# Optimization experiments

Hardware: AMD Instinct MI355X
Metric: run time of the kernel (lower is better)

## Reference

```python
import jax, jax.numpy as jnp
import numpy as np

VOCAB = 50257
D_MODEL = 128
BATCH = 4096
WINDOW = 5  # 2*WINDOW context ids per center word


def setup_inputs() -> dict:
    key = jax.random.key(0)
    k1, k2, k3, k4 = jax.random.split(key, 4)
    context_ids = jax.random.randint(k1, (BATCH, 2 * WINDOW), 0, VOCAB, dtype=jnp.int64 if jax.config.jax_enable_x64 else jnp.int32)
    center_ids = jax.random.randint(k2, (BATCH,), 0, VOCAB, dtype=jnp.int64 if jax.config.jax_enable_x64 else jnp.int32)
    emb = jax.random.normal(k3, (VOCAB, D_MODEL), dtype=jnp.float32)
    W = jax.random.normal(k4, (VOCAB, D_MODEL), dtype=jnp.float32)
    return {"context_ids": context_ids, "center_ids": center_ids, "emb": emb, "W": W}


def reference(context_ids, center_ids, emb, W):
    # CBOW: gather context embeddings, average over the window, project to vocab.
    ctx = emb[context_ids]                      # [B, 2W, D]
    cbow = ctx.mean(axis=1)                     # [B, D]
    logits = jnp.einsum("bd,vd->bv", cbow, W)   # [B, V]
    # CrossEntropyLoss (mean reduction) against center ids.
    logp = jax.nn.log_softmax(logits, axis=-1)  # [B, V]
    nll = -jnp.take_along_axis(logp, center_ids[:, None], axis=-1)[:, 0]
    loss = nll.mean()
    return loss
```

## Files before the change

kernel.cpp:

```cpp
#include <hip/hip_runtime.h>
#include <hip/hip_bf16.h>
#include <math.h>

#define VOCAB 50257
#define VPAD  50304
#define DMODEL 128
#define BATCH 4096
#define NW 10
#define LOG2E 1.4426950408889634f

typedef __bf16 bf16_t;
typedef __bf16 bf16x4 __attribute__((ext_vector_type(4)));
typedef __bf16 bf16x8 __attribute__((ext_vector_type(8)));
typedef float  floatx4 __attribute__((ext_vector_type(4)));

#if __has_builtin(__builtin_amdgcn_exp2f)
#define EXP2(x) __builtin_amdgcn_exp2f(x)
#else
#define EXP2(x) exp2f(x)
#endif

typedef const __attribute__((address_space(1))) void* gvp;
typedef __attribute__((address_space(3))) void* svp;

#define PREP_CBOW_BLOCKS 512
#define PREP_WCONV_BLOCKS 3144

__global__ void k_prep(const int* __restrict__ ctx, const int* __restrict__ center,
                       const float* __restrict__ emb, const float* __restrict__ W,
                       bf16_t* __restrict__ cbow_bf, bf16_t* __restrict__ Wb,
                       float* __restrict__ center_logit, float* __restrict__ sumexp) {
    const int tid = threadIdx.x;
    if (blockIdx.x < PREP_CBOW_BLOCKS) {
        const int g32 = tid >> 5;
        const int l32 = tid & 31;
        const int b = blockIdx.x * 8 + g32;
        const int* cr = ctx + b * NW;
        float4 s = make_float4(0.f, 0.f, 0.f, 0.f);
#pragma unroll
        for (int w = 0; w < NW; ++w) {
            const int id = cr[w];
            float4 v = *reinterpret_cast<const float4*>(emb + (long)id * DMODEL + l32 * 4);
            s.x += v.x; s.y += v.y; s.z += v.z; s.w += v.w;
        }
        s.x *= 0.1f; s.y *= 0.1f; s.z *= 0.1f; s.w *= 0.1f;
        bf16x4 o;
        o[0] = (bf16_t)(s.x * LOG2E); o[1] = (bf16_t)(s.y * LOG2E);
        o[2] = (bf16_t)(s.z * LOG2E); o[3] = (bf16_t)(s.w * LOG2E);
        *reinterpret_cast<bf16x4*>(cbow_bf + b * DMODEL + l32 * 4) = o;

        const int cid = center[b];
        float4 wv = *reinterpret_cast<const float4*>(W + (long)cid * DMODEL + l32 * 4);
        float p = s.x * wv.x + s.y * wv.y + s.z * wv.z + s.w * wv.w;
#pragma unroll
        for (int off = 16; off >= 1; off >>= 1) p += __shfl_xor(p, off, 64);
        if (l32 == 0) {
            center_logit[b] = p;
            sumexp[b] = 0.f;
        }
    } else {
        const long base = ((long)(blockIdx.x - PREP_CBOW_BLOCKS) * 256 + tid) * 8;
        bf16x8 o;
        if (base < (long)VOCAB * DMODEL) {
            float4 a = *reinterpret_cast<const float4*>(W + base);
            float4 b = *reinterpret_cast<const float4*>(W + base + 4);
            o[0] = (bf16_t)a.x; o[1] = (bf16_t)a.y; o[2] = (bf16_t)a.z; o[3] = (bf16_t)a.w;
            o[4] = (bf16_t)b.x; o[5] = (bf16_t)b.y; o[6] = (bf16_t)b.z; o[7] = (bf16_t)b.w;
        } else {
            o = (bf16x8)(bf16_t)0.f;
        }
        *reinterpret_cast<bf16x8*>(Wb + base) = o;
    }
}

#define BM 256
#define BN 128
#define NTILES 393
#define NSPLIT 32

__device__ __forceinline__ void stage_tile(const bf16_t* __restrict__ Wb,
                                           bf16_t* bs, int n0, int wv, int l15, int q) {
#pragma unroll
    for (int i = 0; i < 8; ++i) {
        const int f = wv * 8 + i;
        const int nf = f >> 2, ks = f & 3;
        const bf16_t* g = Wb + (long)(n0 + nf * 16 + l15) * DMODEL + ks * 32 + q * 8;
        __builtin_amdgcn_global_load_lds((gvp)g, (svp)(bs + f * 512), 16, 0, 0);
    }
}

template<bool MASKED>
__device__ __forceinline__ void compute_tile(const bf16_t* bs,
                                             const bf16x8 (&afrag)[4][4],
                                             float (&ssum)[4][4],
                                             int n0, int lane, int l15) {
#pragma unroll
    for (int nf = 0; nf < 8; ++nf) {
        const bf16_t* bp = bs + nf * 2048 + lane * 8;
        bf16x8 b0 = *reinterpret_cast<const bf16x8*>(bp);
        bf16x8 b1 = *reinterpret_cast<const bf16x8*>(bp + 512);
        bf16x8 b2 = *reinterpret_cast<const bf16x8*>(bp + 1024);
        bf16x8 b3 = *reinterpret_cast<const bf16x8*>(bp + 1536);

        floatx4 acc[4];
#pragma unroll
        for (int mf = 0; mf < 4; ++mf) acc[mf] = (floatx4){0.f, 0.f, 0.f, 0.f};
#pragma unroll
        for (int mf = 0; mf < 4; ++mf)
            acc[mf] = __builtin_amdgcn_mfma_f32_16x16x32_bf16(afrag[mf][0], b0, acc[mf], 0, 0, 0);
#pragma unroll
        for (int mf = 0; mf < 4; ++mf)
            acc[mf] = __builtin_amdgcn_mfma_f32_16x16x32_bf16(afrag[mf][1], b1, acc[mf], 0, 0, 0);
#pragma unroll
        for (int mf = 0; mf < 4; ++mf)
            acc[mf] = __builtin_amdgcn_mfma_f32_16x16x32_bf16(afrag[mf][2], b2, acc[mf], 0, 0, 0);
#pragma unroll
        for (int mf = 0; mf < 4; ++mf)
            acc[mf] = __builtin_amdgcn_mfma_f32_16x16x32_bf16(afrag[mf][3], b3, acc[mf], 0, 0, 0);

        const bool ok = !MASKED || ((n0 + nf * 16 + l15) < VOCAB);
#pragma unroll
        for (int mf = 0; mf < 4; ++mf) {
#pragma unroll
            for (int r = 0; r < 4; ++r) {
                float e = EXP2(acc[mf][r]);
                ssum[mf][r] += ok ? e : 0.f;
            }
        }
    }
}

__launch_bounds__(256, 2)
__global__ void k_gemm(const bf16_t* __restrict__ A, const bf16_t* __restrict__ Wb,
                       float* __restrict__ sumexp) {
    __shared__ bf16_t Bs[2][32 * 512];
    const int tid  = threadIdx.x;
    const int lane = tid & 63;
    const int wv   = tid >> 6;
    const int l15  = lane & 15;
    const int q    = lane >> 4;
    const int m0   = blockIdx.x * BM;
    const int by   = blockIdx.y;

    stage_tile(Wb, &Bs[0][0], by * BN, wv, l15, q);

    bf16x8 afrag[4][4];
#pragma unroll
    for (int mf = 0; mf < 4; ++mf) {
        const bf16_t* ap = A + (long)(m0 + wv * 64 + mf * 16 + l15) * DMODEL + q * 8;
#pragma unroll
        for (int ks = 0; ks < 4; ++ks)
            afrag[mf][ks] = *reinterpret_cast<const bf16x8*>(ap + ks * 32);
    }

    float ssum[4][4];
#pragma unroll
    for (int mf = 0; mf < 4; ++mf)
#pragma unroll
        for (int r = 0; r < 4; ++r) ssum[mf][r] = 0.f;

    asm volatile("s_waitcnt vmcnt(0)" ::: "memory");
    __builtin_amdgcn_s_barrier();
    __builtin_amdgcn_sched_barrier(0);

    int cur = 0;
    for (int nt = by; nt < NTILES; nt += NSPLIT) {
        const int nnext = nt + NSPLIT;
        if (nnext < NTILES)
            stage_tile(Wb, &Bs[cur ^ 1][0], nnext * BN, wv, l15, q);

        const int n0 = nt * BN;
        const bf16_t* bs = &Bs[cur][0];
        if (n0 + BN <= VOCAB)
            compute_tile<false>(bs, afrag, ssum, n0, lane, l15);
        else
            compute_tile<true>(bs, afrag, ssum, n0, lane, l15);

        asm volatile("s_waitcnt vmcnt(0)" ::: "memory");
        __builtin_amdgcn_s_barrier();
        __builtin_amdgcn_sched_barrier(0);
        cur ^= 1;
    }

#pragma unroll
    for (int mf = 0; mf < 4; ++mf) {
        float s0 = ssum[mf][0], s1 = ssum[mf][1], s2 = ssum[mf][2], s3 = ssum[mf][3];
#pragma unroll
        for (int off = 1; off < 16; off <<= 1) {
            s0 += __shfl_xor(s0, off, 64);
            s1 += __shfl_xor(s1, off, 64);
            s2 += __shfl_xor(s2, off, 64);
            s3 += __shfl_xor(s3, off, 64);
        }
        if (l15 == 0) {
            const int rbase = m0 + wv * 64 + mf * 16 + q * 4;
            atomicAdd(&sumexp[rbase + 0], s0);
            atomicAdd(&sumexp[rbase + 1], s1);
            atomicAdd(&sumexp[rbase + 2], s2);
            atomicAdd(&sumexp[rbase + 3], s3);
        }
    }
}

__global__ void k_loss(const float* __restrict__ sumexp,
                       const float* __restrict__ center_logit,
                       float* __restrict__ out) {
    float acc = 0.f;
    for (int b = threadIdx.x; b < BATCH; b += 256)
        acc += logf(sumexp[b]) - center_logit[b];
#pragma unroll
    for (int off = 32; off >= 1; off >>= 1) acc += __shfl_xor(acc, off, 64);
    __shared__ float red[4];
    if ((threadIdx.x & 63) == 0) red[threadIdx.x >> 6] = acc;
    __syncthreads();
    if (threadIdx.x == 0)
        out[0] = (red[0] + red[1] + red[2] + red[3]) * (1.0f / BATCH);
}

extern "C" void kernel_launch(void* const* d_in, const int* in_sizes, int n_in,
                              void* d_out, int out_size, void* d_ws, size_t ws_size,
                              hipStream_t stream) {
    const int*   ctx    = (const int*)d_in[0];
    const int*   center = (const int*)d_in[1];
    const float* emb    = (const float*)d_in[2];
    const float* W      = (const float*)d_in[3];
    float*       out    = (float*)d_out;

    char* ws = (char*)d_ws;
    bf16_t* Wb           = (bf16_t*)ws;
    bf16_t* cbow         = (bf16_t*)(ws + 12877824);
    float*  center_logit = (float*)(ws + 13926400);
    float*  sumexp       = (float*)(ws + 13942784);

    k_prep<<<PREP_CBOW_BLOCKS + PREP_WCONV_BLOCKS, 256, 0, stream>>>(
        ctx, center, emb, W, cbow, Wb, center_logit, sumexp);
    dim3 g2(BATCH / BM, NSPLIT);
    k_gemm<<<g2, 256, 0, stream>>>(cbow, Wb, sumexp);
    k_loss<<<1, 256, 0, stream>>>(sumexp, center_logit, out);
}
```

Baseline: 147.3 us.

## Fuse loss reduction into GEMM via last-block counter, shrink N tile, raise occupancy

Removes the separate loss kernel by having the last GEMM block to finish, detected through an atomic counter, compute the final log-sum-exp mean. The N tile drops from 128 to 96 columns and the split count rises to 48. LDS use per block falls, so the launch bound moves to 3 blocks per CU. MFMA sections get raised wave priority, and the grid is flattened to 1D with split-major ordering so blocks sharing an M tile run together. This saves one kernel launch and aims for better latency hiding, at the cost of atomic-read overhead and a serial tail in one block.

```diff
diff --git a/kernel.cpp b/kernel.cpp
--- a/kernel.cpp
+++ b/kernel.cpp
@@ -29,8 +29,10 @@
 __global__ void k_prep(const int* __restrict__ ctx, const int* __restrict__ center,
                        const float* __restrict__ emb, const float* __restrict__ W,
                        bf16_t* __restrict__ cbow_bf, bf16_t* __restrict__ Wb,
-                       float* __restrict__ center_logit, float* __restrict__ sumexp) {
+                       float* __restrict__ center_logit, float* __restrict__ sumexp,
+                       unsigned* __restrict__ cnt) {
     const int tid = threadIdx.x;
+    if (blockIdx.x == 0 && tid == 0) *cnt = 0u;
     if (blockIdx.x < PREP_CBOW_BLOCKS) {
         const int g32 = tid >> 5;
         const int l32 = tid & 31;
@@ -74,15 +76,17 @@
 }
 
 #define BM 256
-#define BN 128
-#define NTILES 393
-#define NSPLIT 32
+#define BN 96
+#define NFRAG 6
+#define NTILES 524
+#define NSPLIT 48
+#define NBLK (16 * NSPLIT)
 
 __device__ __forceinline__ void stage_tile(const bf16_t* __restrict__ Wb,
                                            bf16_t* bs, int n0, int wv, int l15, int q) {
 #pragma unroll
-    for (int i = 0; i < 8; ++i) {
-        const int f = wv * 8 + i;
+    for (int i = 0; i < 6; ++i) {
+        const int f = wv * 6 + i;
         const int nf = f >> 2, ks = f & 3;
         const bf16_t* g = Wb + (long)(n0 + nf * 16 + l15) * DMODEL + ks * 32 + q * 8;
         __builtin_amdgcn_global_load_lds((gvp)g, (svp)(bs + f * 512), 16, 0, 0);
@@ -95,7 +99,7 @@
                                              float (&ssum)[4][4],
                                              int n0, int lane, int l15) {
 #pragma unroll
-    for (int nf = 0; nf < 8; ++nf) {
+    for (int nf = 0; nf < NFRAG; ++nf) {
         const bf16_t* bp = bs + nf * 2048 + lane * 8;
         bf16x8 b0 = *reinterpret_cast<const bf16x8*>(bp);
         bf16x8 b1 = *reinterpret_cast<const bf16x8*>(bp + 512);
@@ -105,6 +109,8 @@
         floatx4 acc[4];
 #pragma unroll
         for (int mf = 0; mf < 4; ++mf) acc[mf] = (floatx4){0.f, 0.f, 0.f, 0.f};
+
+        __builtin_amdgcn_s_setprio(1);
 #pragma unroll
         for (int mf = 0; mf < 4; ++mf)
             acc[mf] = __builtin_amdgcn_mfma_f32_16x16x32_bf16(afrag[mf][0], b0, acc[mf], 0, 0, 0);
@@ -117,6 +123,7 @@
 #pragma unroll
         for (int mf = 0; mf < 4; ++mf)
             acc[mf] = __builtin_amdgcn_mfma_f32_16x16x32_bf16(afrag[mf][3], b3, acc[mf], 0, 0, 0);
+        __builtin_amdgcn_s_setprio(0);
 
         const bool ok = !MASKED || ((n0 + nf * 16 + l15) < VOCAB);
 #pragma unroll
@@ -130,17 +137,23 @@
     }
 }
 
-__launch_bounds__(256, 2)
+__launch_bounds__(256, 3)
 __global__ void k_gemm(const bf16_t* __restrict__ A, const bf16_t* __restrict__ Wb,
-                       float* __restrict__ sumexp) {
-    __shared__ bf16_t Bs[2][32 * 512];
+                       float* __restrict__ sumexp,
+                       const float* __restrict__ center_logit,
+                       float* __restrict__ out, unsigned* __restrict__ cnt) {
+    __shared__ bf16_t Bs[2][24 * 512];
+    __shared__ float red[4];
+    __shared__ unsigned lastflag;
     const int tid  = threadIdx.x;
     const int lane = tid & 63;
     const int wv   = tid >> 6;
     const int l15  = lane & 15;
     const int q    = lane >> 4;
-    const int m0   = blockIdx.x * BM;
-    const int by   = blockIdx.y;
+    const int lin  = blockIdx.x;
+    const int bx   = lin / NSPLIT;
+    const int by   = lin % NSPLIT;
+    const int m0   = bx * BM;
 
     stage_tile(Wb, &Bs[0][0], by * BN, wv, l15, q);
 
@@ -200,21 +213,27 @@
             atomicAdd(&sumexp[rbase + 3], s3);
         }
     }
-}
-
-__global__ void k_loss(const float* __restrict__ sumexp,
-                       const float* __restrict__ center_logit,
-                       float* __restrict__ out) {
-    float acc = 0.f;
-    for (int b = threadIdx.x; b < BATCH; b += 256)
-        acc += logf(sumexp[b]) - center_logit[b];
-#pragma unroll
-    for (int off = 32; off >= 1; off >>= 1) acc += __shfl_xor(acc, off, 64);
-    __shared__ float red[4];
-    if ((threadIdx.x & 63) == 0) red[threadIdx.x >> 6] = acc;
+
     __syncthreads();
-    if (threadIdx.x == 0)
-        out[0] = (red[0] + red[1] + red[2] + red[3]) * (1.0f / BATCH);
+    if (tid == 0) {
+        unsigned v = __hip_atomic_fetch_add(cnt, 1u, __ATOMIC_ACQ_REL,
+                                            __HIP_MEMORY_SCOPE_AGENT);
+        lastflag = (v == NBLK - 1) ? 1u : 0u;
+    }
+    __syncthreads();
+    if (lastflag) {
+        float acc = 0.f;
+        for (int b = tid; b < BATCH; b += 256) {
+            float se = atomicAdd(&sumexp[b], 0.0f);
+            acc += logf(se) - center_logit[b];
+        }
+#pragma unroll
+        for (int off = 32; off >= 1; off >>= 1) acc += __shfl_xor(acc, off, 64);
+        if ((tid & 63) == 0) red[tid >> 6] = acc;
+        __syncthreads();
+        if (tid == 0)
+            out[0] = (red[0] + red[1] + red[2] + red[3]) * (1.0f / BATCH);
+    }
 }
 
 extern "C" void kernel_launch(void* const* d_in, const int* in_sizes, int n_in,
@@ -227,14 +246,13 @@
     float*       out    = (float*)d_out;
 
     char* ws = (char*)d_ws;
-    bf16_t* Wb           = (bf16_t*)ws;
-    bf16_t* cbow         = (bf16_t*)(ws + 12877824);
-    float*  center_logit = (float*)(ws + 13926400);
-    float*  sumexp       = (float*)(ws + 13942784);
+    bf16_t*   Wb           = (bf16_t*)ws;
+    bf16_t*   cbow         = (bf16_t*)(ws + 12877824);
+    float*    center_logit = (float*)(ws + 13926400);
+    float*    sumexp       = (float*)(ws + 13942784);
+    unsigned* cnt          = (unsigned*)(ws + 13959168);
 
     k_prep<<<PREP_CBOW_BLOCKS + PREP_WCONV_BLOCKS, 256, 0, stream>>>(
-        ctx, center, emb, W, cbow, Wb, center_logit, sumexp);
-    dim3 g2(BATCH / BM, NSPLIT);
-    k_gemm<<<g2, 256, 0, stream>>>(cbow, Wb, sumexp);
-    k_loss<<<1, 256, 0, stream>>>(sumexp, center_logit, out);
-}
+        ctx, center, emb, W, cbow, Wb, center_logit, sumexp, cnt);
+    k_gemm<<<NBLK, 256, 0, stream>>>(cbow, Wb, sumexp, center_logit, out, cnt);
+}
```

After: 270.0 us. +83.3%, slower.
